# Optimization experiments

Measured on AMD Instinct MI355X. Metric: run time of the kernel, lower is better.

## Reference

```python
import jax, jax.numpy as jnp
import numpy as np

B, S, E, U, V, C = 128, 256, 128, 512, 50257, 3


def _lstm(xs, Wk, Wr, b):
    """Single LSTM layer over time. xs: [S, B, D] -> hs: [S, B, U].
    Keras LSTMCell gate order i, f, g(c), o; sigmoid recurrent activation, tanh activation."""
    Bd = xs.shape[1]
    Ud = Wr.shape[0]
    def step(carry, x):
        h, c = carry
        z = x @ Wk + h @ Wr + b          # [B, 4U]
        i, f, g, o = jnp.split(z, 4, axis=-1)
        c = jax.nn.sigmoid(f) * c + jax.nn.sigmoid(i) * jnp.tanh(g)
        h = jax.nn.sigmoid(o) * jnp.tanh(c)
        return (h, c), h
    init = (jnp.zeros((Bd, Ud), xs.dtype), jnp.zeros((Bd, Ud), xs.dtype))
    _, hs = jax.lax.scan(step, init, xs)
    return hs


def setup_inputs() -> dict:
    key = jax.random.key(0)
    ks = jax.random.split(key, 16)
    def p(k, shape, scale=0.05):
        return (jax.random.normal(k, shape) * scale).astype(jnp.float32)
    inp = {}
    inp["tokens"] = jax.random.randint(ks[0], (B, S), 0, V + 1)
    inp["emb"] = p(ks[1], (V + 1, E))
    i = 2
    for name, d_in in (("fw0", E), ("fw1", U), ("bw0", E), ("bw1", U)):
        inp[f"{name}_Wk"] = p(ks[i], (d_in, 4 * U)); i += 1
        inp[f"{name}_Wr"] = p(ks[i], (U, 4 * U)); i += 1
        inp[f"{name}_b"] = jnp.zeros((4 * U,), jnp.float32)
    inp["dense_W"] = p(ks[i], (2 * U, C))
    inp["dense_b"] = jnp.zeros((C,), jnp.float32)
    return inp


def reference(tokens, emb,
              fw0_Wk, fw0_Wr, fw0_b, fw1_Wk, fw1_Wr, fw1_b,
              bw0_Wk, bw0_Wr, bw0_b, bw1_Wk, bw1_Wr, bw1_b,
              dense_W, dense_b):
    x = emb[tokens]                      # [B, S, E]
    xs = jnp.transpose(x, (1, 0, 2))     # [S, B, E] time-major for scan
    # forward stacked RNN: layer0 -> layer1
    fw = _lstm(_lstm(xs, fw0_Wk, fw0_Wr, fw0_b), fw1_Wk, fw1_Wr, fw1_b)
    # backward stacked RNN: reversed input, output re-reversed to align in time
    xr = xs[::-1]
    bw = _lstm(_lstm(xr, bw0_Wk, bw0_Wr, bw0_b), bw1_Wk, bw1_Wr, bw1_b)[::-1]
    h = jnp.concatenate([fw, bw], axis=-1)          # [S, B, 2U]
    h = jnp.transpose(h, (1, 0, 2))                 # [B, S, 2U]
    return jax.nn.softmax(h @ dense_W + dense_b, axis=-1)  # [B, S, C]
```

## Files before the change

### kernel.cpp

```cpp
#include <hip/hip_runtime.h>
#include <hip/hip_bf16.h>

typedef unsigned short u16;
typedef unsigned int u32;
typedef unsigned long long u64;
typedef __attribute__((ext_vector_type(8))) short s16x8;
typedef __attribute__((ext_vector_type(4))) float f32x4;

static constexpr size_t OFF_CNT = 0;
static constexpr size_t OFF_H0  = 8192;
static constexpr size_t OFF_H1  = OFF_H0 + 1048576;
static constexpr size_t OFF_LOG = OFF_H1 + 1048576;
static constexpr size_t ZB      = OFF_LOG + 393216;
static constexpr size_t OFF_X   = ZB;
static constexpr size_t OFF_W   = OFF_X + 8388608;
static constexpr size_t CB_FW0 = 0;
static constexpr size_t CB_FW1 = 1327104;
static constexpr size_t CB_BW0 = 3440640;
static constexpr size_t CB_BW1 = 4767744;
static constexpr unsigned SMEM_BYTES = 64 * 1032 * 2 + 4 * 512;

__device__ inline u16 f2bu(float f) {
    union { float f; u32 u; } v; v.f = f;
    u32 x = v.u;
    return (u16)((x + 0x7fffu + ((x >> 16) & 1u)) >> 16);
}
__device__ inline float sigf(float x) {
    x = fminf(fmaxf(x, -30.f), 30.f);
    return 1.f / (1.f + __expf(-x));
}
__device__ inline float tanh_f(float x) {
    x = fminf(fmaxf(x, -15.f), 15.f);
    float e = __expf(2.f * x);
    return (e - 1.f) / (e + 1.f);
}

__global__ void embed_k(const int* __restrict__ tokens, const float2* __restrict__ emb,
                        u32* __restrict__ Xo) {
    int sb = blockIdx.x;
    int b = sb & 127, s = sb >> 7;
    int tok = tokens[b * 256 + s];
    float2 v = emb[(size_t)tok * 64 + threadIdx.x];
    Xo[(size_t)sb * 64 + threadIdx.x] = (u32)f2bu(v.x) | ((u32)f2bu(v.y) << 16);
}

__global__ void wrepack_k(const float* __restrict__ Wr, const float* __restrict__ Wk,
                          u16* __restrict__ dst, int Kc) {
    int e = blockIdx.x * 256 + threadIdx.x;
    int krow = e % Kc;
    int nn = e / Kc;
    if (nn >= 2048) return;
    int i = nn >> 6, n = nn & 63;
    int g = n >> 4, u = n & 15;
    int col = g * 512 + i * 16 + u;
    float v = (krow < 512) ? Wr[(size_t)krow * 2048 + col]
                           : Wk[(size_t)(krow - 512) * 2048 + col];
    dst[(size_t)nn * (Kc + 8) + krow] = f2bu(v);
}

__device__ inline void wait2(int* a, int* b) {
    if (threadIdx.x == 0) {
        int spins = 0;
        bool oka = (a == nullptr), okb = (b == nullptr);
        while (!(oka && okb)) {
            if (!oka) oka = __hip_atomic_load(a, __ATOMIC_RELAXED, __HIP_MEMORY_SCOPE_AGENT) >= 32;
            if (!okb) okb = __hip_atomic_load(b, __ATOMIC_RELAXED, __HIP_MEMORY_SCOPE_AGENT) >= 32;
            if (oka && okb) break;
            __builtin_amdgcn_s_sleep(2);
            if (++spins > (1 << 17)) break;
        }
        __builtin_amdgcn_fence(__ATOMIC_ACQUIRE, "agent");
    }
    __syncthreads();
}

template <int LAYER>
__device__ __forceinline__ void run_chain(
    const u16* __restrict__ wlds, u16* __restrict__ tlds, const u16* __restrict__ X,
    u16* __restrict__ H0, u16* __restrict__ H1, int* __restrict__ cb,
    float* __restrict__ logits, const float* __restrict__ bptr,
    const float* __restrict__ dW,
    int dir, int p, int strip, int wv, int lane)
{
    constexpr int Kpad = LAYER ? 1032 : 648;
    const int tid  = threadIdx.x;
    const int uu   = lane & 15;
    const int qq   = lane >> 4;
    const int rowA = p * 64 + wv * 16 + uu;
    const u16* blds = wlds + (size_t)uu * Kpad + qq * 8;

    float bias[4];
#pragma unroll
    for (int g = 0; g < 4; ++g) bias[g] = bptr[g * 512 + strip * 16 + uu];
    float wd[3] = {0.f, 0.f, 0.f};
    if (LAYER == 1) {
#pragma unroll
        for (int c = 0; c < 3; ++c)
            wd[c] = dW[(size_t)(dir * 512 + strip * 16 + uu) * 3 + c];
    }

    float cst[4] = {0.f, 0.f, 0.f, 0.f};

    for (int t = 0; t < 256; ++t) {
        s16x8 af[16], af2[16], xf[4];

        if (LAYER == 0) {
            int tx = dir ? (255 - t) : t;
            const u16* xb = X + (size_t)tx * 16384 + rowA * 128 + qq * 8;
#pragma unroll
            for (int j = 0; j < 4; ++j) xf[j] = *(const s16x8*)(xb + j * 32);

            int* fa = (t > 0)  ? &cb[(0 * 256 + (t - 1)) * 2 + p] : nullptr;
            int* fb = (t >= 4) ? &cb[(256 + (t - 4)) * 2 + p]     : nullptr;
            if (fa || fb) wait2(fa, fb);

            const u16* pa = H0 + ((t - 1) & 3) * 65536 + (size_t)rowA * 512 + qq * 8;
#pragma unroll
            for (int i = 0; i < 16; ++i) af[i] = *(const s16x8*)(pa + i * 32);
        } else {
            int* fa = &cb[(0 * 256 + t) * 2 + p];
            int* fb = (t > 0) ? &cb[(256 + (t - 1)) * 2 + p] : nullptr;
            wait2(fa, fb);

            const u16* pb = H0 + (t & 3) * 65536 + (size_t)rowA * 512 + qq * 8;
#pragma unroll
            for (int i = 0; i < 16; ++i) af2[i] = *(const s16x8*)(pb + i * 32);
            const u16* pa = H1 + ((t - 1) & 3) * 65536 + (size_t)rowA * 512 + qq * 8;
#pragma unroll
            for (int i = 0; i < 16; ++i) af[i] = *(const s16x8*)(pa + i * 32);
        }

        f32x4 acc[4];
#pragma unroll
        for (int g = 0; g < 4; ++g)
            acc[g] = (f32x4){bias[g], bias[g], bias[g], bias[g]};

#pragma unroll
        for (int kt = 0; kt < 16; ++kt) {
            s16x8 av = af[kt];
#pragma unroll
            for (int g = 0; g < 4; ++g) {
                s16x8 bv = *(const s16x8*)(blds + (size_t)g * 16 * Kpad + kt * 32);
                acc[g] = __builtin_amdgcn_mfma_f32_16x16x32_bf16(av, bv, acc[g], 0, 0, 0);
            }
        }
        if (LAYER == 0) {
#pragma unroll
            for (int j = 0; j < 4; ++j) {
                s16x8 av = xf[j];
#pragma unroll
                for (int g = 0; g < 4; ++g) {
                    s16x8 bv = *(const s16x8*)(blds + (size_t)g * 16 * Kpad + (16 + j) * 32);
                    acc[g] = __builtin_amdgcn_mfma_f32_16x16x32_bf16(av, bv, acc[g], 0, 0, 0);
                }
            }
        } else {
#pragma unroll
            for (int kt = 0; kt < 16; ++kt) {
                s16x8 av = af2[kt];
#pragma unroll
                for (int g = 0; g < 4; ++g) {
                    s16x8 bv = *(const s16x8*)(blds + (size_t)g * 16 * Kpad + (16 + kt) * 32);
                    acc[g] = __builtin_amdgcn_mfma_f32_16x16x32_bf16(av, bv, acc[g], 0, 0, 0);
                }
            }
        }

        u16* Hout = (LAYER == 0) ? H0 + (t & 3) * 65536 : H1 + (t & 3) * 65536;
        float hv[4];
        u32 hb[4];
#pragma unroll
        for (int j = 0; j < 4; ++j) {
            float iv = sigf(acc[0][j]);
            float fv = sigf(acc[1][j]);
            float gv = tanh_f(acc[2][j]);
            float ov = sigf(acc[3][j]);
            float cj = fv * cst[j] + iv * gv;
            cst[j] = cj;
            float h = ov * tanh_f(cj);
            hv[j] = h;
            hb[j] = (u32)f2bu(h);
        }

        u16* tw = tlds + wv * 256;
#pragma unroll
        for (int j = 0; j < 4; ++j)
            tw[(qq * 4 + j) * 16 + uu] = (u16)hb[j];
        asm volatile("s_waitcnt lgkmcnt(0)" ::: "memory");
        __builtin_amdgcn_sched_barrier(0);
        {
            const int r  = lane >> 2;
            const int cq = lane & 3;
            u64 v = *(const u64*)(tw + r * 16 + cq * 4);
            u16* dst = Hout + (size_t)(p * 64 + wv * 16 + r) * 512 + strip * 16 + cq * 4;
            asm volatile("global_store_dwordx2 %0, %1, off sc0 sc1"
                         :: "v"(dst), "v"(v) : "memory");
        }

        asm volatile("s_waitcnt vmcnt(0)" ::: "memory");
        __syncthreads();
        if (tid == 0)
            __hip_atomic_fetch_add(&cb[(LAYER * 256 + t) * 2 + p], 1,
                                   __ATOMIC_RELAXED, __HIP_MEMORY_SCOPE_AGENT);

        if (LAYER == 1) {
            int s_out = dir ? (255 - t) : t;
            const int rowC = p * 64 + wv * 16 + qq * 4;
#pragma unroll
            for (int j = 0; j < 4; ++j) {
#pragma unroll
                for (int c = 0; c < 3; ++c) {
                    float v = hv[j] * wd[c];
                    v += __shfl_xor(v, 1);
                    v += __shfl_xor(v, 2);
                    v += __shfl_xor(v, 4);
                    v += __shfl_xor(v, 8);
                    if (uu == 0)
                        atomicAdd(&logits[((size_t)(rowC + j) * 256 + s_out) * 3 + c], v);
                }
            }
        }
    }
    asm volatile("s_waitcnt vmcnt(0)" ::: "memory");
}

__global__ void __launch_bounds__(256, 1)
lstm_engine(const u16* __restrict__ Wg, const u16* __restrict__ X,
            u16* __restrict__ h0ring, u16* __restrict__ h1ring,
            int* __restrict__ cnt, float* __restrict__ logits,
            const float* __restrict__ bf0, const float* __restrict__ bf1,
            const float* __restrict__ bb0, const float* __restrict__ bb1,
            const float* __restrict__ dW) {
    extern __shared__ u16 wlds[];
    const int tid = threadIdx.x;
    const int bid = blockIdx.x;
    const int dir   = bid >> 7;
    const int rr    = bid & 127;
    const int layer = rr >> 6;
    const int q     = rr & 63;
    const int strip = q >> 1;
    const int p     = q & 1;
    const int wv    = tid >> 6;
    const int lane  = tid & 63;

    const int Kc   = layer ? 1024 : 640;
    const int Kpad = Kc + 8;
    const size_t cbase = layer ? (dir ? CB_BW1 : CB_FW1) : (dir ? CB_BW0 : CB_FW0);
    const u16* wsrc = Wg + cbase + (size_t)strip * 64 * Kpad;

    {
        const uint4* s4 = (const uint4*)wsrc;
        uint4* d4 = (uint4*)wlds;
        const int n16 = (64 * Kpad) / 8;
        for (int j = tid; j < n16; j += 256) d4[j] = s4[j];
    }
    __syncthreads();

    u16* tlds = wlds + (size_t)64 * Kpad;

    u16* H0 = h0ring + (size_t)dir * (4 * 65536);
    u16* H1 = h1ring + (size_t)dir * (4 * 65536);
    int* cb = cnt + dir * (2 * 256 * 2);
    const float* bptr = layer ? (dir ? bb1 : bf1) : (dir ? bb0 : bf0);

    if (layer == 0)
        run_chain<0>(wlds, tlds, X, H0, H1, cb, logits, bptr, dW, dir, p, strip, wv, lane);
    else
        run_chain<1>(wlds, tlds, X, H0, H1, cb, logits, bptr, dW, dir, p, strip, wv, lane);
}

__global__ void softmax_k(const float* __restrict__ logits, const float* __restrict__ db,
                          float* __restrict__ out) {
    int idx = blockIdx.x * 256 + threadIdx.x;
    float l0 = logits[(size_t)idx * 3 + 0] + db[0];
    float l1 = logits[(size_t)idx * 3 + 1] + db[1];
    float l2 = logits[(size_t)idx * 3 + 2] + db[2];
    float m = fmaxf(l0, fmaxf(l1, l2));
    float e0 = __expf(l0 - m), e1 = __expf(l1 - m), e2 = __expf(l2 - m);
    float r = 1.f / (e0 + e1 + e2);
    out[(size_t)idx * 3 + 0] = e0 * r;
    out[(size_t)idx * 3 + 1] = e1 * r;
    out[(size_t)idx * 3 + 2] = e2 * r;
}

extern "C" void kernel_launch(void* const* d_in, const int* in_sizes, int n_in,
                              void* d_out, int out_size, void* d_ws, size_t ws_size,
                              hipStream_t stream) {
    (void)in_sizes; (void)n_in; (void)out_size; (void)ws_size;
    const int*    tokens = (const int*)d_in[0];
    const float2* emb    = (const float2*)d_in[1];
    const float* fw0_Wk = (const float*)d_in[2];
    const float* fw0_Wr = (const float*)d_in[3];
    const float* fw0_b  = (const float*)d_in[4];
    const float* fw1_Wk = (const float*)d_in[5];
    const float* fw1_Wr = (const float*)d_in[6];
    const float* fw1_b  = (const float*)d_in[7];
    const float* bw0_Wk = (const float*)d_in[8];
    const float* bw0_Wr = (const float*)d_in[9];
    const float* bw0_b  = (const float*)d_in[10];
    const float* bw1_Wk = (const float*)d_in[11];
    const float* bw1_Wr = (const float*)d_in[12];
    const float* bw1_b  = (const float*)d_in[13];
    const float* dW     = (const float*)d_in[14];
    const float* db     = (const float*)d_in[15];

    char* ws = (char*)d_ws;
    int*   cnt = (int*)(ws + OFF_CNT);
    u16*   H0  = (u16*)(ws + OFF_H0);
    u16*   H1  = (u16*)(ws + OFF_H1);
    float* lg  = (float*)(ws + OFF_LOG);
    u32*   Xw  = (u32*)(ws + OFF_X);
    const u16* Xr = (const u16*)(ws + OFF_X);
    u16*   Wg  = (u16*)(ws + OFF_W);
    const u16* Wgc = Wg;

    hipMemsetAsync(ws, 0, ZB, stream);
    embed_k<<<32768, 64, 0, stream>>>(tokens, emb, Xw);
    wrepack_k<<<5120, 256, 0, stream>>>(fw0_Wr, fw0_Wk, Wg + CB_FW0, 640);
    wrepack_k<<<8192, 256, 0, stream>>>(fw1_Wr, fw1_Wk, Wg + CB_FW1, 1024);
    wrepack_k<<<5120, 256, 0, stream>>>(bw0_Wr, bw0_Wk, Wg + CB_BW0, 640);
    wrepack_k<<<8192, 256, 0, stream>>>(bw1_Wr, bw1_Wk, Wg + CB_BW1, 1024);

    hipFuncSetAttribute((const void*)lstm_engine,
                        hipFuncAttributeMaxDynamicSharedMemorySize, SMEM_BYTES);
    void* args[] = { (void*)&Wgc, (void*)&Xr, (void*)&H0, (void*)&H1, (void*)&cnt,
                     (void*)&lg, (void*)&fw0_b, (void*)&fw1_b, (void*)&bw0_b,
                     (void*)&bw1_b, (void*)&dW };
    hipLaunchCooperativeKernel((const void*)lstm_engine, dim3(256), dim3(256),
                               args, SMEM_BYTES, stream);

    softmax_k<<<128, 256, 0, stream>>>(lg, db, (float*)d_out);
}
```

Baseline: 2.784 ms.

## Overlap input-side MFMAs with flag waits and signal per-wave instead of per-block

Moves the input-projection MFMAs (embedding x for layer 0, H0 contribution for layer 1 when its flag is already complete) ahead of the recurrent-dependency wait, so useful work overlaps the spin on the previous step's flags. The block-wide __syncthreads before the flag increment is dropped: each wave increments the counter itself, and the ready threshold rises from 32 to 128 to count waves instead of blocks. This shortens the critical path of the sequential recurrence, at the cost of extra branches, more counter atomics, and a memory-ordering risk from releasing per wave without a fence.

```diff
diff --git a/kernel.cpp b/kernel.cpp
--- a/kernel.cpp
+++ b/kernel.cpp
@@ -20,6 +20,8 @@
 static constexpr size_t CB_BW1 = 4767744;
 static constexpr unsigned SMEM_BYTES = 64 * 1032 * 2 + 4 * 512;
 
+static constexpr int FLAG_FULL = 128;
+
 __device__ inline u16 f2bu(float f) {
     union { float f; u32 u; } v; v.f = f;
     u32 x = v.u;
@@ -63,8 +65,8 @@
         int spins = 0;
         bool oka = (a == nullptr), okb = (b == nullptr);
         while (!(oka && okb)) {
-            if (!oka) oka = __hip_atomic_load(a, __ATOMIC_RELAXED, __HIP_MEMORY_SCOPE_AGENT) >= 32;
-            if (!okb) okb = __hip_atomic_load(b, __ATOMIC_RELAXED, __HIP_MEMORY_SCOPE_AGENT) >= 32;
+            if (!oka) oka = __hip_atomic_load(a, __ATOMIC_RELAXED, __HIP_MEMORY_SCOPE_AGENT) >= FLAG_FULL;
+            if (!okb) okb = __hip_atomic_load(b, __ATOMIC_RELAXED, __HIP_MEMORY_SCOPE_AGENT) >= FLAG_FULL;
             if (oka && okb) break;
             __builtin_amdgcn_s_sleep(2);
             if (++spins > (1 << 17)) break;
@@ -83,7 +85,6 @@
     int dir, int p, int strip, int wv, int lane)
 {
     constexpr int Kpad = LAYER ? 1032 : 648;
-    const int tid  = threadIdx.x;
     const int uu   = lane & 15;
     const int qq   = lane >> 4;
     const int rowA = p * 64 + wv * 16 + uu;
@@ -103,12 +104,25 @@
 
     for (int t = 0; t < 256; ++t) {
         s16x8 af[16], af2[16], xf[4];
+        f32x4 acc[4];
+#pragma unroll
+        for (int g = 0; g < 4; ++g)
+            acc[g] = (f32x4){bias[g], bias[g], bias[g], bias[g]};
 
         if (LAYER == 0) {
             int tx = dir ? (255 - t) : t;
             const u16* xb = X + (size_t)tx * 16384 + rowA * 128 + qq * 8;
 #pragma unroll
             for (int j = 0; j < 4; ++j) xf[j] = *(const s16x8*)(xb + j * 32);
+#pragma unroll
+            for (int j = 0; j < 4; ++j) {
+                s16x8 av = xf[j];
+#pragma unroll
+                for (int g = 0; g < 4; ++g) {
+                    s16x8 bv = *(const s16x8*)(blds + (size_t)g * 16 * Kpad + (16 + j) * 32);
+                    acc[g] = __builtin_amdgcn_mfma_f32_16x16x32_bf16(av, bv, acc[g], 0, 0, 0);
+                }
+            }
 
             int* fa = (t > 0)  ? &cb[(0 * 256 + (t - 1)) * 2 + p] : nullptr;
             int* fb = (t >= 4) ? &cb[(256 + (t - 4)) * 2 + p]     : nullptr;
@@ -117,51 +131,65 @@
             const u16* pa = H0 + ((t - 1) & 3) * 65536 + (size_t)rowA * 512 + qq * 8;
 #pragma unroll
             for (int i = 0; i < 16; ++i) af[i] = *(const s16x8*)(pa + i * 32);
+#pragma unroll
+            for (int kt = 0; kt < 16; ++kt) {
+                s16x8 av = af[kt];
+#pragma unroll
+                for (int g = 0; g < 4; ++g) {
+                    s16x8 bv = *(const s16x8*)(blds + (size_t)g * 16 * Kpad + kt * 32);
+                    acc[g] = __builtin_amdgcn_mfma_f32_16x16x32_bf16(av, bv, acc[g], 0, 0, 0);
+                }
+            }
         } else {
             int* fa = &cb[(0 * 256 + t) * 2 + p];
             int* fb = (t > 0) ? &cb[(256 + (t - 1)) * 2 + p] : nullptr;
+
+            int fv = 0;
+            if (lane == 0)
+                fv = __hip_atomic_load(fa, __ATOMIC_RELAXED, __HIP_MEMORY_SCOPE_AGENT);
+            fv = __shfl(fv, 0);
+            const bool h0r = (fv >= FLAG_FULL);
+
+            const u16* pb = H0 + (t & 3) * 65536 + (size_t)rowA * 512 + qq * 8;
+            if (h0r) {
+#pragma unroll
+                for (int i = 0; i < 16; ++i) af2[i] = *(const s16x8*)(pb + i * 32);
+#pragma unroll
+                for (int kt = 0; kt < 16; ++kt) {
+                    s16x8 av = af2[kt];
+#pragma unroll
+                    for (int g = 0; g < 4; ++g) {
+                        s16x8 bv = *(const s16x8*)(blds + (size_t)g * 16 * Kpad + (16 + kt) * 32);
+                        acc[g] = __builtin_amdgcn_mfma_f32_16x16x32_bf16(av, bv, acc[g], 0, 0, 0);
+                    }
+                }
+            }
+
             wait2(fa, fb);
 
-            const u16* pb = H0 + (t & 3) * 65536 + (size_t)rowA * 512 + qq * 8;
-#pragma unroll
-            for (int i = 0; i < 16; ++i) af2[i] = *(const s16x8*)(pb + i * 32);
             const u16* pa = H1 + ((t - 1) & 3) * 65536 + (size_t)rowA * 512 + qq * 8;
 #pragma unroll
             for (int i = 0; i < 16; ++i) af[i] = *(const s16x8*)(pa + i * 32);
-        }
-
-        f32x4 acc[4];
-#pragma unroll
-        for (int g = 0; g < 4; ++g)
-            acc[g] = (f32x4){bias[g], bias[g], bias[g], bias[g]};
-
-#pragma unroll
-        for (int kt = 0; kt < 16; ++kt) {
-            s16x8 av = af[kt];
-#pragma unroll
-            for (int g = 0; g < 4; ++g) {
-                s16x8 bv = *(const s16x8*)(blds + (size_t)g * 16 * Kpad + kt * 32);
-                acc[g] = __builtin_amdgcn_mfma_f32_16x16x32_bf16(av, bv, acc[g], 0, 0, 0);
-            }
-        }
-        if (LAYER == 0) {
-#pragma unroll
-            for (int j = 0; j < 4; ++j) {
-                s16x8 av = xf[j];
+#pragma unroll
+            for (int kt = 0; kt < 16; ++kt) {
+                s16x8 av = af[kt];
 #pragma unroll
                 for (int g = 0; g < 4; ++g) {
-                    s16x8 bv = *(const s16x8*)(blds + (size_t)g * 16 * Kpad + (16 + j) * 32);
+                    s16x8 bv = *(const s16x8*)(blds + (size_t)g * 16 * Kpad + kt * 32);
                     acc[g] = __builtin_amdgcn_mfma_f32_16x16x32_bf16(av, bv, acc[g], 0, 0, 0);
                 }
             }
-        } else {
-#pragma unroll
-            for (int kt = 0; kt < 16; ++kt) {
-                s16x8 av = af2[kt];
-#pragma unroll
-                for (int g = 0; g < 4; ++g) {
-                    s16x8 bv = *(const s16x8*)(blds + (size_t)g * 16 * Kpad + (16 + kt) * 32);
-                    acc[g] = __builtin_amdgcn_mfma_f32_16x16x32_bf16(av, bv, acc[g], 0, 0, 0);
+            if (!h0r) {
+#pragma unroll
+                for (int i = 0; i < 16; ++i) af2[i] = *(const s16x8*)(pb + i * 32);
+#pragma unroll
+                for (int kt = 0; kt < 16; ++kt) {
+                    s16x8 av = af2[kt];
+#pragma unroll
+                    for (int g = 0; g < 4; ++g) {
+                        s16x8 bv = *(const s16x8*)(blds + (size_t)g * 16 * Kpad + (16 + kt) * 32);
+                        acc[g] = __builtin_amdgcn_mfma_f32_16x16x32_bf16(av, bv, acc[g], 0, 0, 0);
+                    }
                 }
             }
         }
@@ -172,10 +200,10 @@
 #pragma unroll
         for (int j = 0; j < 4; ++j) {
             float iv = sigf(acc[0][j]);
-            float fv = sigf(acc[1][j]);
+            float fv2 = sigf(acc[1][j]);
             float gv = tanh_f(acc[2][j]);
             float ov = sigf(acc[3][j]);
-            float cj = fv * cst[j] + iv * gv;
+            float cj = fv2 * cst[j] + iv * gv;
             cst[j] = cj;
             float h = ov * tanh_f(cj);
             hv[j] = h;
@@ -198,8 +226,7 @@
         }
 
         asm volatile("s_waitcnt vmcnt(0)" ::: "memory");
-        __syncthreads();
-        if (tid == 0)
+        if (lane == 0)
             __hip_atomic_fetch_add(&cb[(LAYER * 256 + t) * 2 + p], 1,
                                    __ATOMIC_RELAXED, __HIP_MEMORY_SCOPE_AGENT);
 
```

New measurement: 2.851 ms. 2.4% more time.
